# Kernel optimization log

Measured on AMD Instinct MI355X. Metric: run time of the kernel, lower is better.

Reference implementation:

```python
import jax, jax.numpy as jnp
import numpy as np

ALPHA = 1.0
STRIDE = 1
PAD = 1
DIL = 1


def setup_inputs() -> dict:
    key = jax.random.key(0)
    k1, k2, k3, k4 = jax.random.split(key, 4)
    B, C_in, C_out, H, W, K = 8, 64, 64, 128, 128, 3
    n = C_in * K * K
    stdv = 1.0 / np.sqrt(n)
    x = jax.random.normal(k1, (B, C_in, H, W), dtype=jnp.float32)
    depth = jax.random.uniform(k2, (B, 1, H, W), dtype=jnp.float32)
    weight = jax.random.uniform(k3, (C_out, C_in, K, K), dtype=jnp.float32,
                                minval=-stdv, maxval=stdv)
    bias = jax.random.uniform(k4, (C_out,), dtype=jnp.float32,
                              minval=-stdv, maxval=stdv)
    return {"x": x, "depth": depth, "weight": weight, "bias": bias}


def reference(x, depth, weight, bias):
    # Depth-guided convolution:
    #   out[b,o,p0] = bias[o] + sum_{c,k} W[o,c,k] * x[b,c,p0+pk] * exp(-alpha*|D(p0)-D(p0+pk)|)
    B, C, H, W = x.shape
    O, _, KH, KW = weight.shape
    H_out = (H + 2 * PAD - (DIL * (KH - 1) + 1)) // STRIDE + 1
    W_out = (W + 2 * PAD - (DIL * (KW - 1) + 1)) // STRIDE + 1
    x_p = jnp.pad(x, ((0, 0), (0, 0), (PAD, PAD), (PAD, PAD)))
    d_p = jnp.pad(depth, ((0, 0), (0, 0), (PAD, PAD), (PAD, PAD)))

    def tap(a, kh, kw):
        h0, w0 = kh * DIL, kw * DIL
        return a[:, :, h0:h0 + (H_out - 1) * STRIDE + 1:STRIDE,
                 w0:w0 + (W_out - 1) * STRIDE + 1:STRIDE]

    # depth at the center of each receptive field (kernel assumed odd)
    d_center = tap(d_p, KH // 2, KW // 2)  # [B,1,Ho,Wo]

    out = jnp.zeros((B, O, H_out, W_out), dtype=x.dtype)
    for kh in range(KH):
        for kw in range(KW):
            xs = tap(x_p, kh, kw)                                  # [B,C,Ho,Wo]
            ds = tap(d_p, kh, kw)                                  # [B,1,Ho,Wo]
            sim = jnp.exp(-ALPHA * jnp.abs(ds - d_center))         # [B,1,Ho,Wo]
            out = out + jnp.einsum('oc,bchw->bohw', weight[:, :, kh, kw], xs * sim)
    return out + bias[None, :, None, None]
```

## Files before the change

kernel.cpp:

```cpp
#include <hip/hip_runtime.h>

#define B_ 8
#define C_ 64
#define O_ 64
#define H_ 128
#define W_ 128

typedef __attribute__((ext_vector_type(8))) short bf16x8;
typedef __attribute__((ext_vector_type(4))) float f32x4;

__device__ __forceinline__ unsigned short f2bf(float v) {
    unsigned u = __float_as_uint(v);
    return (unsigned short)((u + 0x7FFFu + ((u >> 16) & 1u)) >> 16);
}

__device__ __forceinline__ int swz(int col) {
    return ((col ^ (col >> 3)) & 7) << 4;
}

__global__ void prep_weights(const float* __restrict__ weight,
                             unsigned short* __restrict__ wfrag) {
    int idx = blockIdx.x * 256 + threadIdx.x;
    if (idx >= 9 * 4096) return;
    int j  = idx & 7;
    int l  = (idx >> 3) & 63;
    int fi = (idx >> 9) & 3;
    int ks = (idx >> 11) & 1;
    int t  = idx >> 12;
    int o  = fi * 16 + (l & 15);
    int c  = ks * 32 + ((l >> 4) & 3) * 8 + j;
    wfrag[idx] = f2bf(weight[(o * C_ + c) * 9 + t]);
}

__global__ __launch_bounds__(256, 2)
void depthconv_mfma4(const float* __restrict__ x,
                     const float* __restrict__ depth,
                     const unsigned short* __restrict__ wfrag,
                     const float* __restrict__ bias,
                     float* __restrict__ out) {
    __shared__ __align__(16) unsigned char xs[396 * 128];
    __shared__ __align__(16) float sim[9][4][64];
    __shared__ __align__(16) float dt[6][68];

    const int tid = threadIdx.x;
    const int blk = blockIdx.x;
    const int b   = blk >> 6;
    const int rem = blk & 63;
    const int h0  = (rem >> 1) * 4;
    const int w0  = (rem & 1) * 64;

    for (int i = tid; i < 396; i += 256) {
        int r = i / 66, col = i - r * 66;
        int gh = h0 - 1 + r, gw = w0 - 1 + col;
        bool ok = ((unsigned)gh < (unsigned)H_) && ((unsigned)gw < (unsigned)W_);
        int ghc = gh < 0 ? 0 : (gh > H_ - 1 ? H_ - 1 : gh);
        int gwc = gw < 0 ? 0 : (gw > W_ - 1 ? W_ - 1 : gw);
        float v = depth[(b * H_ + ghc) * W_ + gwc];
        dt[r][col] = ok ? v : 0.f;
    }
    __syncthreads();

    const int crb = tid >> 4;
    const int q   = tid & 15;
    float4 xv[24];
    #pragma unroll
    for (int k = 0; k < 24; ++k) {
        int idx = crb + 16 * k;
        int c = idx & 63, r = idx >> 6;
        int gh  = h0 - 1 + r;
        int ghc = gh < 0 ? 0 : (gh > H_ - 1 ? H_ - 1 : gh);
        xv[k] = *(const float4*)&x[((b * C_ + c) * H_ + ghc) * W_ + w0 + q * 4];
    }
    float hv[3];
    #pragma unroll
    for (int k = 0; k < 3; ++k) {
        int i = tid + 256 * k;
        int side = i & 1, cr = i >> 1;
        int c = cr & 63, r = cr >> 6;
        int gh = h0 - 1 + r;
        int gw = side ? (w0 + 64) : (w0 - 1);
        bool ok = ((unsigned)gh < (unsigned)H_) && ((unsigned)gw < (unsigned)W_);
        int ghc = gh < 0 ? 0 : (gh > H_ - 1 ? H_ - 1 : gh);
        int gwc = gw < 0 ? 0 : (gw > W_ - 1 ? W_ - 1 : gw);
        float v = x[((b * C_ + c) * H_ + ghc) * W_ + gwc];
        hv[k] = ok ? v : 0.f;
    }

    {
        int hr = (tid >> 6) & 3, px = tid & 63;
        float dc = dt[hr + 1][px + 1];
        #pragma unroll
        for (int t = 0; t < 9; ++t) {
            const int kh = t / 3, kw = t % 3;
            sim[t][hr][px] = expf(-fabsf(dt[hr + kh][px + kw] - dc));
        }
    }

    #pragma unroll
    for (int k = 0; k < 24; ++k) {
        int idx = crb + 16 * k;
        int c = idx & 63, r = idx >> 6;
        int gh = h0 - 1 + r;
        bool okh = (unsigned)gh < (unsigned)H_;
        float vv[4] = {xv[k].x, xv[k].y, xv[k].z, xv[k].w};
        #pragma unroll
        for (int m = 0; m < 4; ++m) {
            int col = 1 + q * 4 + m;
            int rc  = r * 66 + col;
            unsigned short bv = okh ? f2bf(vv[m]) : (unsigned short)0;
            *(unsigned short*)(xs + rc * 128 + ((2 * c) ^ swz(col))) = bv;
        }
    }
    #pragma unroll
    for (int k = 0; k < 3; ++k) {
        int i = tid + 256 * k;
        int side = i & 1, cr = i >> 1;
        int c = cr & 63, r = cr >> 6;
        int col = side ? 65 : 0;
        int rc  = r * 66 + col;
        *(unsigned short*)(xs + rc * 128 + ((2 * c) ^ swz(col))) = f2bf(hv[k]);
    }
    __syncthreads();

    const int lane = tid & 63;
    const int hr   = tid >> 6;
    const int g    = lane >> 4;
    const int ln   = lane & 15;

    float acc[4][4][4];
    #pragma unroll
    for (int of = 0; of < 4; ++of) {
        float bv = bias[of * 16 + ln];
        #pragma unroll
        for (int pf = 0; pf < 4; ++pf)
            #pragma unroll
            for (int r = 0; r < 4; ++r)
                acc[pf][of][r] = bv;
    }

    #pragma unroll 1
    for (int kh = 0; kh < 3; ++kh) {
        #pragma unroll
        for (int kw = 0; kw < 3; ++kw) {
            const int t = kh * 3 + kw;
            bf16x8 bfr[2][4];
            #pragma unroll
            for (int ks = 0; ks < 2; ++ks)
                #pragma unroll
                for (int of = 0; of < 4; ++of)
                    bfr[ks][of] = *(const bf16x8*)(
                        wfrag + (((t * 2 + ks) * 4 + of) * 64 + lane) * 8);

            #pragma unroll
            for (int pf = 0; pf < 4; ++pf) {
                int col = pf * 16 + ln + kw;
                int rcb = (hr + kh) * 66 + col;
                const unsigned char* rowp = xs + rcb * 128;
                bf16x8 af0 = *(const bf16x8*)(rowp + ((2 * (g * 8))      ^ swz(col)));
                bf16x8 af1 = *(const bf16x8*)(rowp + ((2 * (32 + g * 8)) ^ swz(col)));

                f32x4 prt[4] = {};
                #pragma unroll
                for (int of = 0; of < 4; ++of)
                    prt[of] = __builtin_amdgcn_mfma_f32_16x16x32_bf16(
                        af0, bfr[0][of], prt[of], 0, 0, 0);
                #pragma unroll
                for (int of = 0; of < 4; ++of)
                    prt[of] = __builtin_amdgcn_mfma_f32_16x16x32_bf16(
                        af1, bfr[1][of], prt[of], 0, 0, 0);

                f32x4 sv = *(const f32x4*)&sim[t][hr][pf * 16 + g * 4];
                #pragma unroll
                for (int of = 0; of < 4; ++of)
                    #pragma unroll
                    for (int r = 0; r < 4; ++r)
                        acc[pf][of][r] = fmaf(sv[r], prt[of][r], acc[pf][of][r]);
            }
        }
    }

    const int h = h0 + hr;
    #pragma unroll
    for (int of = 0; of < 4; ++of) {
        int o = of * 16 + ln;
        float* dst = out + (((size_t)(b * O_ + o) * H_ + h) * W_) + w0;
        #pragma unroll
        for (int pf = 0; pf < 4; ++pf) {
            f32x4 v = { acc[pf][of][0], acc[pf][of][1],
                        acc[pf][of][2], acc[pf][of][3] };
            *(f32x4*)(dst + pf * 16 + g * 4) = v;
        }
    }
}

extern "C" void kernel_launch(void* const* d_in, const int* in_sizes, int n_in,
                              void* d_out, int out_size, void* d_ws, size_t ws_size,
                              hipStream_t stream) {
    const float* x      = (const float*)d_in[0];
    const float* depth  = (const float*)d_in[1];
    const float* weight = (const float*)d_in[2];
    const float* bias   = (const float*)d_in[3];
    float* out          = (float*)d_out;
    unsigned short* wfrag = (unsigned short*)d_ws;

    prep_weights<<<dim3(144), dim3(256), 0, stream>>>(weight, wfrag);
    depthconv_mfma4<<<dim3(512), dim3(256), 0, stream>>>(
        x, depth, wfrag, bias, out);
}
```

Measured before the change: 37.07 us.

## Halve spatial tile width, raise occupancy, pack channel pairs, remap blocks

Narrows each block's tile from 4x64 to 4x32 output pixels and doubles the grid to 1024 blocks. Launch bounds go from 2 to 4 blocks per CU, and the shared-memory footprint shrinks to match. Each thread now loads two adjacent channels and writes packed bf16x2 values to LDS. Blocks are remapped so consecutive block IDs spread across batch images, the tap loop is fully unrolled, and depth loads are issued before the x loads to overlap latency. The aim is more resident waves to hide global load latency, at the cost of more halo overhead and more redundant loads per output.

New measurement: 88.86 us. 2.4x slower.

```diff
diff --git a/kernel.cpp b/kernel.cpp
--- a/kernel.cpp
+++ b/kernel.cpp
@@ -1,4 +1,5 @@
 #include <hip/hip_runtime.h>
+#include <hip/hip_bf16.h>
 
 #define B_ 8
 #define C_ 64
@@ -32,93 +33,107 @@
     wfrag[idx] = f2bf(weight[(o * C_ + c) * 9 + t]);
 }
 
-__global__ __launch_bounds__(256, 2)
-void depthconv_mfma4(const float* __restrict__ x,
+__global__ __launch_bounds__(256, 4)
+void depthconv_mfma5(const float* __restrict__ x,
                      const float* __restrict__ depth,
                      const unsigned short* __restrict__ wfrag,
                      const float* __restrict__ bias,
                      float* __restrict__ out) {
-    __shared__ __align__(16) unsigned char xs[396 * 128];
-    __shared__ __align__(16) float sim[9][4][64];
-    __shared__ __align__(16) float dt[6][68];
+    __shared__ __align__(16) unsigned char xs[204 * 128];
+    __shared__ __align__(16) float sim[9][4][32];
+    __shared__ __align__(16) float dt[6][36];
 
     const int tid = threadIdx.x;
-    const int blk = blockIdx.x;
-    const int b   = blk >> 6;
-    const int rem = blk & 63;
-    const int h0  = (rem >> 1) * 4;
-    const int w0  = (rem & 1) * 64;
-
-    for (int i = tid; i < 396; i += 256) {
-        int r = i / 66, col = i - r * 66;
-        int gh = h0 - 1 + r, gw = w0 - 1 + col;
+    const int blk = (blockIdx.x & 7) * 128 + (blockIdx.x >> 3);
+    const int b   = blk >> 7;
+    const int rem = blk & 127;
+    const int h0  = (rem >> 2) * 4;
+    const int w0  = (rem & 3) * 32;
+
+    float dv = 0.f;
+    int dr = 0, dcol = 0;
+    if (tid < 216) {
+        dr = tid / 36; dcol = tid - dr * 36;
+        int gh = h0 - 1 + dr, gw = w0 - 1 + dcol;
         bool ok = ((unsigned)gh < (unsigned)H_) && ((unsigned)gw < (unsigned)W_);
         int ghc = gh < 0 ? 0 : (gh > H_ - 1 ? H_ - 1 : gh);
         int gwc = gw < 0 ? 0 : (gw > W_ - 1 ? W_ - 1 : gw);
         float v = depth[(b * H_ + ghc) * W_ + gwc];
-        dt[r][col] = ok ? v : 0.f;
-    }
+        dv = ok ? v : 0.f;
+    }
+
+    const int q   = tid & 7;
+    const int pcr = tid >> 3;
+    const int c0p = 2 * pcr;
+    float4 xa[6], xb[6];
+    bool okh[6];
+    #pragma unroll
+    for (int r = 0; r < 6; ++r) {
+        int gh = h0 - 1 + r;
+        okh[r] = (unsigned)gh < (unsigned)H_;
+        int ghc = gh < 0 ? 0 : (gh > H_ - 1 ? H_ - 1 : gh);
+        const float* base = &x[((b * C_ + c0p) * H_ + ghc) * W_ + w0 + q * 4];
+        xa[r] = *(const float4*)base;
+        xb[r] = *(const float4*)(base + H_ * W_);
+    }
+    float hl0[2], hl1[2];
+    int hside[2], hcp[2], hr_[2];
+    bool hok[2];
+    #pragma unroll
+    for (int k = 0; k < 2; ++k) {
+        int i = tid + 256 * k;
+        hok[k] = false;
+        if (i < 384) {
+            int side = i & 1, rp = i >> 1;
+            int cp = rp & 31, r = rp >> 5;
+            hside[k] = side; hcp[k] = cp; hr_[k] = r;
+            int gh = h0 - 1 + r;
+            int gw = side ? (w0 + 32) : (w0 - 1);
+            bool ok = ((unsigned)gh < (unsigned)H_) && ((unsigned)gw < (unsigned)W_);
+            hok[k] = true;
+            int ghc = gh < 0 ? 0 : (gh > H_ - 1 ? H_ - 1 : gh);
+            int gwc = gw < 0 ? 0 : (gw > W_ - 1 ? W_ - 1 : gw);
+            const float* p = &x[((b * C_ + 2 * cp) * H_ + ghc) * W_ + gwc];
+            float v0 = p[0], v1 = p[H_ * W_];
+            hl0[k] = ok ? v0 : 0.f;
+            hl1[k] = ok ? v1 : 0.f;
+        }
+    }
+
+    if (tid < 216) dt[dr][dcol] = dv;
     __syncthreads();
-
-    const int crb = tid >> 4;
-    const int q   = tid & 15;
-    float4 xv[24];
-    #pragma unroll
-    for (int k = 0; k < 24; ++k) {
-        int idx = crb + 16 * k;
-        int c = idx & 63, r = idx >> 6;
-        int gh  = h0 - 1 + r;
-        int ghc = gh < 0 ? 0 : (gh > H_ - 1 ? H_ - 1 : gh);
-        xv[k] = *(const float4*)&x[((b * C_ + c) * H_ + ghc) * W_ + w0 + q * 4];
-    }
-    float hv[3];
-    #pragma unroll
-    for (int k = 0; k < 3; ++k) {
-        int i = tid + 256 * k;
-        int side = i & 1, cr = i >> 1;
-        int c = cr & 63, r = cr >> 6;
-        int gh = h0 - 1 + r;
-        int gw = side ? (w0 + 64) : (w0 - 1);
-        bool ok = ((unsigned)gh < (unsigned)H_) && ((unsigned)gw < (unsigned)W_);
-        int ghc = gh < 0 ? 0 : (gh > H_ - 1 ? H_ - 1 : gh);
-        int gwc = gw < 0 ? 0 : (gw > W_ - 1 ? W_ - 1 : gw);
-        float v = x[((b * C_ + c) * H_ + ghc) * W_ + gwc];
-        hv[k] = ok ? v : 0.f;
-    }
-
-    {
-        int hr = (tid >> 6) & 3, px = tid & 63;
-        float dc = dt[hr + 1][px + 1];
-        #pragma unroll
-        for (int t = 0; t < 9; ++t) {
-            const int kh = t / 3, kw = t % 3;
-            sim[t][hr][px] = expf(-fabsf(dt[hr + kh][px + kw] - dc));
-        }
-    }
-
-    #pragma unroll
-    for (int k = 0; k < 24; ++k) {
-        int idx = crb + 16 * k;
-        int c = idx & 63, r = idx >> 6;
-        int gh = h0 - 1 + r;
-        bool okh = (unsigned)gh < (unsigned)H_;
-        float vv[4] = {xv[k].x, xv[k].y, xv[k].z, xv[k].w};
+    for (int i = tid; i < 1152; i += 256) {
+        int t  = i >> 7;
+        int hr = (i >> 5) & 3;
+        int px = i & 31;
+        int kh = t / 3, kw = t - kh * 3;
+        sim[t][hr][px] = expf(-fabsf(dt[hr + kh][px + kw] - dt[hr + 1][px + 1]));
+    }
+
+    #pragma unroll
+    for (int r = 0; r < 6; ++r) {
+        float va[4] = {xa[r].x, xa[r].y, xa[r].z, xa[r].w};
+        float vb[4] = {xb[r].x, xb[r].y, xb[r].z, xb[r].w};
         #pragma unroll
         for (int m = 0; m < 4; ++m) {
             int col = 1 + q * 4 + m;
-            int rc  = r * 66 + col;
-            unsigned short bv = okh ? f2bf(vv[m]) : (unsigned short)0;
-            *(unsigned short*)(xs + rc * 128 + ((2 * c) ^ swz(col))) = bv;
-        }
-    }
-    #pragma unroll
-    for (int k = 0; k < 3; ++k) {
-        int i = tid + 256 * k;
-        int side = i & 1, cr = i >> 1;
-        int c = cr & 63, r = cr >> 6;
-        int col = side ? 65 : 0;
-        int rc  = r * 66 + col;
-        *(unsigned short*)(xs + rc * 128 + ((2 * c) ^ swz(col))) = f2bf(hv[k]);
+            int rc  = r * 34 + col;
+            float2 pr;
+            pr.x = okh[r] ? va[m] : 0.f;
+            pr.y = okh[r] ? vb[m] : 0.f;
+            __hip_bfloat162 bv = __float22bfloat162_rn(pr);
+            *(__hip_bfloat162*)(xs + rc * 128 + ((4 * pcr) ^ swz(col))) = bv;
+        }
+    }
+    #pragma unroll
+    for (int k = 0; k < 2; ++k) {
+        if (hok[k]) {
+            int col = hside[k] ? 33 : 0;
+            int rc  = hr_[k] * 34 + col;
+            float2 pr; pr.x = hl0[k]; pr.y = hl1[k];
+            __hip_bfloat162 bv = __float22bfloat162_rn(pr);
+            *(__hip_bfloat162*)(xs + rc * 128 + ((4 * hcp[k]) ^ swz(col))) = bv;
+        }
     }
     __syncthreads();
 
@@ -127,55 +142,52 @@
     const int g    = lane >> 4;
     const int ln   = lane & 15;
 
-    float acc[4][4][4];
+    float acc[2][4][4];
     #pragma unroll
     for (int of = 0; of < 4; ++of) {
         float bv = bias[of * 16 + ln];
         #pragma unroll
-        for (int pf = 0; pf < 4; ++pf)
+        for (int pf = 0; pf < 2; ++pf)
             #pragma unroll
             for (int r = 0; r < 4; ++r)
                 acc[pf][of][r] = bv;
     }
 
-    #pragma unroll 1
-    for (int kh = 0; kh < 3; ++kh) {
-        #pragma unroll
-        for (int kw = 0; kw < 3; ++kw) {
-            const int t = kh * 3 + kw;
-            bf16x8 bfr[2][4];
-            #pragma unroll
-            for (int ks = 0; ks < 2; ++ks)
+    #pragma unroll
+    for (int t = 0; t < 9; ++t) {
+        const int kh = t / 3, kw = t - (t / 3) * 3;
+        bf16x8 bfr[2][4];
+        #pragma unroll
+        for (int ks = 0; ks < 2; ++ks)
+            #pragma unroll
+            for (int of = 0; of < 4; ++of)
+                bfr[ks][of] = *(const bf16x8*)(
+                    wfrag + (((t * 2 + ks) * 4 + of) * 64 + lane) * 8);
+
+        #pragma unroll
+        for (int pf = 0; pf < 2; ++pf) {
+            int col = pf * 16 + ln + kw;
+            int rcb = (hr + kh) * 34 + col;
+            const unsigned char* rowp = xs + rcb * 128;
+            bf16x8 af0 = *(const bf16x8*)(rowp + ((16 * g) ^ swz(col)));
+            bf16x8 af1 = *(const bf16x8*)(rowp + ((64 + 16 * g) ^ swz(col)));
+
+            f32x4 prt[4] = {};
+            #pragma unroll
+            for (int of = 0; of < 4; ++of)
+                prt[of] = __builtin_amdgcn_mfma_f32_16x16x32_bf16(
+                    af0, bfr[0][of], prt[of], 0, 0, 0);
+            #pragma unroll
+            for (int of = 0; of < 4; ++of)
+                prt[of] = __builtin_amdgcn_mfma_f32_16x16x32_bf16(
+                    af1, bfr[1][of], prt[of], 0, 0, 0);
+
+            f32x4 sv = *(const f32x4*)&sim[t][hr][pf * 16 + g * 4];
+            #pragma unroll
+            for (int of = 0; of < 4; ++of)
                 #pragma unroll
-                for (int of = 0; of < 4; ++of)
-                    bfr[ks][of] = *(const bf16x8*)(
-                        wfrag + (((t * 2 + ks) * 4 + of) * 64 + lane) * 8);
-
-            #pragma unroll
-            for (int pf = 0; pf < 4; ++pf) {
-                int col = pf * 16 + ln + kw;
-                int rcb = (hr + kh) * 66 + col;
-                const unsigned char* rowp = xs + rcb * 128;
-                bf16x8 af0 = *(const bf16x8*)(rowp + ((2 * (g * 8))      ^ swz(col)));
-                bf16x8 af1 = *(const bf16x8*)(rowp + ((2 * (32 + g * 8)) ^ swz(col)));
-
-                f32x4 prt[4] = {};
-                #pragma unroll
-                for (int of = 0; of < 4; ++of)
-                    prt[of] = __builtin_amdgcn_mfma_f32_16x16x32_bf16(
-                        af0, bfr[0][of], prt[of], 0, 0, 0);
-                #pragma unroll
-                for (int of = 0; of < 4; ++of)
-                    prt[of] = __builtin_amdgcn_mfma_f32_16x16x32_bf16(
-                        af1, bfr[1][of], prt[of], 0, 0, 0);
-
-                f32x4 sv = *(const f32x4*)&sim[t][hr][pf * 16 + g * 4];
-                #pragma unroll
-                for (int of = 0; of < 4; ++of)
-                    #pragma unroll
-                    for (int r = 0; r < 4; ++r)
-                        acc[pf][of][r] = fmaf(sv[r], prt[of][r], acc[pf][of][r]);
-            }
+                for (int r = 0; r < 4; ++r)
+                    acc[pf][of][r] = fmaf(sv[r], prt[of][r], acc[pf][of][r]);
         }
     }
 
@@ -185,7 +197,7 @@
         int o = of * 16 + ln;
         float* dst = out + (((size_t)(b * O_ + o) * H_ + h) * W_) + w0;
         #pragma unroll
-        for (int pf = 0; pf < 4; ++pf) {
+        for (int pf = 0; pf < 2; ++pf) {
             f32x4 v = { acc[pf][of][0], acc[pf][of][1],
                         acc[pf][of][2], acc[pf][of][3] };
             *(f32x4*)(dst + pf * 16 + g * 4) = v;
@@ -204,6 +216,6 @@
     unsigned short* wfrag = (unsigned short*)d_ws;
 
     prep_weights<<<dim3(144), dim3(256), 0, stream>>>(weight, wfrag);
-    depthconv_mfma4<<<dim3(512), dim3(256), 0, stream>>>(
+    depthconv_mfma5<<<dim3(1024), dim3(256), 0, stream>>>(
         x, depth, wfrag, bias, out);
 }
```

## Stage output tile through LDS for coalesced stores and pack bf16 pairs

Applied to the files above, without the earlier changes.

Shared memory becomes one 64KB arena that holds the input tile, sim and depth, and is reused at the end to stage the output accumulators. Threads then write full contiguous 256-byte rows per output channel and row, where before they issued scattered 16-byte stores. The x staging now loads channel pairs and converts them with a packed bf16x2 conversion, writing 4-byte LDS stores instead of 2-byte ones. The costs are a larger LDS footprint, which may limit the 2-blocks-per-CU occupancy, and extra barriers plus an LDS round trip in the epilogue.

After: 36.59 us. Within noise of the previous version (-1.3%).

```diff
diff --git a/kernel.cpp b/kernel.cpp
--- a/kernel.cpp
+++ b/kernel.cpp
@@ -1,4 +1,5 @@
 #include <hip/hip_runtime.h>
+#include <hip/hip_bf16.h>
 
 #define B_ 8
 #define C_ 64
@@ -33,14 +34,15 @@
 }
 
 __global__ __launch_bounds__(256, 2)
-void depthconv_mfma4(const float* __restrict__ x,
+void depthconv_mfma6(const float* __restrict__ x,
                      const float* __restrict__ depth,
                      const unsigned short* __restrict__ wfrag,
                      const float* __restrict__ bias,
                      float* __restrict__ out) {
-    __shared__ __align__(16) unsigned char xs[396 * 128];
-    __shared__ __align__(16) float sim[9][4][64];
-    __shared__ __align__(16) float dt[6][68];
+    __shared__ __align__(16) unsigned char arena[65536];
+    unsigned char* xs   = arena;
+    float (*sim)[4][64] = (float (*)[4][64])(arena + 50688);
+    float (*dt)[68]     = (float (*)[68])(arena + 59904);
 
     const int tid = threadIdx.x;
     const int blk = blockIdx.x;
@@ -60,65 +62,81 @@
     }
     __syncthreads();
 
-    const int crb = tid >> 4;
-    const int q   = tid & 15;
-    float4 xv[24];
-    #pragma unroll
-    for (int k = 0; k < 24; ++k) {
-        int idx = crb + 16 * k;
-        int c = idx & 63, r = idx >> 6;
-        int gh  = h0 - 1 + r;
-        int ghc = gh < 0 ? 0 : (gh > H_ - 1 ? H_ - 1 : gh);
-        xv[k] = *(const float4*)&x[((b * C_ + c) * H_ + ghc) * W_ + w0 + q * 4];
-    }
-    float hv[3];
-    #pragma unroll
-    for (int k = 0; k < 3; ++k) {
+    const int q  = tid & 15;
+    const int pc = tid >> 4;
+    float4 xa[12], xb[12];
+    #pragma unroll
+    for (int k = 0; k < 12; ++k) {
+        int r    = k >> 1;
+        int pair = pc + 16 * (k & 1);
+        int gh   = h0 - 1 + r;
+        int ghc  = gh < 0 ? 0 : (gh > H_ - 1 ? H_ - 1 : gh);
+        const float* base = &x[((b * C_ + 2 * pair) * H_ + ghc) * W_ + w0 + q * 4];
+        xa[k] = *(const float4*)base;
+        xb[k] = *(const float4*)(base + H_ * W_);
+    }
+    float hl0[2], hl1[2];
+    int hside[2], hpair[2], hr_[2];
+    bool hact[2];
+    #pragma unroll
+    for (int k = 0; k < 2; ++k) {
         int i = tid + 256 * k;
-        int side = i & 1, cr = i >> 1;
-        int c = cr & 63, r = cr >> 6;
-        int gh = h0 - 1 + r;
-        int gw = side ? (w0 + 64) : (w0 - 1);
-        bool ok = ((unsigned)gh < (unsigned)H_) && ((unsigned)gw < (unsigned)W_);
-        int ghc = gh < 0 ? 0 : (gh > H_ - 1 ? H_ - 1 : gh);
-        int gwc = gw < 0 ? 0 : (gw > W_ - 1 ? W_ - 1 : gw);
-        float v = x[((b * C_ + c) * H_ + ghc) * W_ + gwc];
-        hv[k] = ok ? v : 0.f;
+        hact[k] = false;
+        if (i < 384) {
+            int side = i & 1, rp = i >> 1;
+            int pair = rp & 31, r = rp >> 5;
+            hside[k] = side; hpair[k] = pair; hr_[k] = r;
+            hact[k] = true;
+            int gh = h0 - 1 + r;
+            int gw = side ? (w0 + 64) : (w0 - 1);
+            bool ok = ((unsigned)gh < (unsigned)H_) && ((unsigned)gw < (unsigned)W_);
+            int ghc = gh < 0 ? 0 : (gh > H_ - 1 ? H_ - 1 : gh);
+            int gwc = gw < 0 ? 0 : (gw > W_ - 1 ? W_ - 1 : gw);
+            const float* p = &x[((b * C_ + 2 * pair) * H_ + ghc) * W_ + gwc];
+            float v0 = p[0], v1 = p[H_ * W_];
+            hl0[k] = ok ? v0 : 0.f;
+            hl1[k] = ok ? v1 : 0.f;
+        }
     }
 
     {
-        int hr = (tid >> 6) & 3, px = tid & 63;
-        float dc = dt[hr + 1][px + 1];
+        int shr = (tid >> 6) & 3, px = tid & 63;
+        float dc = dt[shr + 1][px + 1];
         #pragma unroll
         for (int t = 0; t < 9; ++t) {
             const int kh = t / 3, kw = t % 3;
-            sim[t][hr][px] = expf(-fabsf(dt[hr + kh][px + kw] - dc));
-        }
-    }
-
-    #pragma unroll
-    for (int k = 0; k < 24; ++k) {
-        int idx = crb + 16 * k;
-        int c = idx & 63, r = idx >> 6;
-        int gh = h0 - 1 + r;
+            sim[t][shr][px] = expf(-fabsf(dt[shr + kh][px + kw] - dc));
+        }
+    }
+
+    #pragma unroll
+    for (int k = 0; k < 12; ++k) {
+        int r    = k >> 1;
+        int pair = pc + 16 * (k & 1);
+        int gh   = h0 - 1 + r;
         bool okh = (unsigned)gh < (unsigned)H_;
-        float vv[4] = {xv[k].x, xv[k].y, xv[k].z, xv[k].w};
+        float va[4] = {xa[k].x, xa[k].y, xa[k].z, xa[k].w};
+        float vb[4] = {xb[k].x, xb[k].y, xb[k].z, xb[k].w};
         #pragma unroll
         for (int m = 0; m < 4; ++m) {
             int col = 1 + q * 4 + m;
             int rc  = r * 66 + col;
-            unsigned short bv = okh ? f2bf(vv[m]) : (unsigned short)0;
-            *(unsigned short*)(xs + rc * 128 + ((2 * c) ^ swz(col))) = bv;
-        }
-    }
-    #pragma unroll
-    for (int k = 0; k < 3; ++k) {
-        int i = tid + 256 * k;
-        int side = i & 1, cr = i >> 1;
-        int c = cr & 63, r = cr >> 6;
-        int col = side ? 65 : 0;
-        int rc  = r * 66 + col;
-        *(unsigned short*)(xs + rc * 128 + ((2 * c) ^ swz(col))) = f2bf(hv[k]);
+            float2 pr;
+            pr.x = okh ? va[m] : 0.f;
+            pr.y = okh ? vb[m] : 0.f;
+            __hip_bfloat162 bv = __float22bfloat162_rn(pr);
+            *(__hip_bfloat162*)(xs + rc * 128 + ((4 * pair) ^ swz(col))) = bv;
+        }
+    }
+    #pragma unroll
+    for (int k = 0; k < 2; ++k) {
+        if (hact[k]) {
+            int col = hside[k] ? 65 : 0;
+            int rc  = hr_[k] * 66 + col;
+            float2 pr; pr.x = hl0[k]; pr.y = hl1[k];
+            __hip_bfloat162 bv = __float22bfloat162_rn(pr);
+            *(__hip_bfloat162*)(xs + rc * 128 + ((4 * hpair[k]) ^ swz(col))) = bv;
+        }
     }
     __syncthreads();
 
@@ -156,8 +174,8 @@
                 int col = pf * 16 + ln + kw;
                 int rcb = (hr + kh) * 66 + col;
                 const unsigned char* rowp = xs + rcb * 128;
-                bf16x8 af0 = *(const bf16x8*)(rowp + ((2 * (g * 8))      ^ swz(col)));
-                bf16x8 af1 = *(const bf16x8*)(rowp + ((2 * (32 + g * 8)) ^ swz(col)));
+                bf16x8 af0 = *(const bf16x8*)(rowp + ((16 * g) ^ swz(col)));
+                bf16x8 af1 = *(const bf16x8*)(rowp + ((64 + 16 * g) ^ swz(col)));
 
                 f32x4 prt[4] = {};
                 #pragma unroll
@@ -179,17 +197,28 @@
         }
     }
 
-    const int h = h0 + hr;
-    #pragma unroll
-    for (int of = 0; of < 4; ++of) {
-        int o = of * 16 + ln;
-        float* dst = out + (((size_t)(b * O_ + o) * H_ + h) * W_) + w0;
-        #pragma unroll
-        for (int pf = 0; pf < 4; ++pf) {
+    __syncthreads();
+    #pragma unroll
+    for (int pf = 0; pf < 4; ++pf)
+        #pragma unroll
+        for (int of = 0; of < 4; ++of) {
+            int rowid = ((of * 16 + ln) << 2) + hr;
+            int chunk = (pf << 2) + g;
             f32x4 v = { acc[pf][of][0], acc[pf][of][1],
                         acc[pf][of][2], acc[pf][of][3] };
-            *(f32x4*)(dst + pf * 16 + g * 4) = v;
-        }
+            *(f32x4*)(arena + rowid * 256 + ((chunk ^ ln) << 4)) = v;
+        }
+    __syncthreads();
+    #pragma unroll
+    for (int m = 0; m < 16; ++m) {
+        int idx   = m * 256 + tid;
+        int rowid = idx >> 4;
+        int cc    = idx & 15;
+        int key   = (rowid >> 2) & 15;
+        f32x4 v = *(const f32x4*)(arena + rowid * 256 + ((cc ^ key) << 4));
+        int o  = rowid >> 2;
+        int hh = rowid & 3;
+        *(f32x4*)(out + (((size_t)(b * O_ + o) * H_ + h0 + hh) * W_) + w0 + cc * 4) = v;
     }
 }
 
@@ -204,6 +233,6 @@
     unsigned short* wfrag = (unsigned short*)d_ws;
 
     prep_weights<<<dim3(144), dim3(256), 0, stream>>>(weight, wfrag);
-    depthconv_mfma4<<<dim3(512), dim3(256), 0, stream>>>(
+    depthconv_mfma6<<<dim3(512), dim3(256), 0, stream>>>(
         x, depth, wfrag, bias, out);
 }
```

## Split 64-wide tile into two 32-wide halves with prefetch of second half

Applied to the files above, without the earlier changes.

Each block now stages its 64-column tile in two 32-column halves through a smaller shared buffer. The second half's global loads are issued before the first half's MFMA compute, so load latency overlaps with math. Channels are packed in pairs and written as bf16x2 to shared memory. The smaller LDS footprint may allow more resident blocks, at the cost of an extra barrier, the weight fragments being reloaded per half, and more live registers for the prefetched data.

After: 44.09 us. +18.9%, slower.

```diff
diff --git a/kernel.cpp b/kernel.cpp
--- a/kernel.cpp
+++ b/kernel.cpp
@@ -1,10 +1,12 @@
 #include <hip/hip_runtime.h>
+#include <hip/hip_bf16.h>
 
 #define B_ 8
 #define C_ 64
 #define O_ 64
 #define H_ 128
 #define W_ 128
+#define HW_ (H_ * W_)
 
 typedef __attribute__((ext_vector_type(8))) short bf16x8;
 typedef __attribute__((ext_vector_type(4))) float f32x4;
@@ -13,9 +15,11 @@
     unsigned u = __float_as_uint(v);
     return (unsigned short)((u + 0x7FFFu + ((u >> 16) & 1u)) >> 16);
 }
-
 __device__ __forceinline__ int swz(int col) {
     return ((col ^ (col >> 3)) & 7) << 4;
+}
+__device__ __forceinline__ int clampi(int v, int lo, int hi) {
+    return v < lo ? lo : (v > hi ? hi : v);
 }
 
 __global__ void prep_weights(const float* __restrict__ weight,
@@ -32,163 +36,246 @@
     wfrag[idx] = f2bf(weight[(o * C_ + c) * 9 + t]);
 }
 
+template<int SB>
+__device__ __forceinline__ void compute_tile(
+    const unsigned char* xs, const float (&sim)[9][4][64],
+    const unsigned short* __restrict__ wfrag,
+    int hr, int g, int ln, int lane, float (&acc)[2][4][4]) {
+    #pragma unroll 1
+    for (int kh = 0; kh < 3; ++kh) {
+        #pragma unroll
+        for (int kw = 0; kw < 3; ++kw) {
+            const int t = kh * 3 + kw;
+            bf16x8 bfr[2][4];
+            #pragma unroll
+            for (int ks = 0; ks < 2; ++ks)
+                #pragma unroll
+                for (int of = 0; of < 4; ++of)
+                    bfr[ks][of] = *(const bf16x8*)(
+                        wfrag + (((t * 2 + ks) * 4 + of) * 64 + lane) * 8);
+
+            #pragma unroll
+            for (int pf = 0; pf < 2; ++pf) {
+                int col = pf * 16 + ln + kw;
+                const unsigned char* rowp = xs + ((hr + kh) * 34 + col) * 128;
+                bf16x8 af0 = *(const bf16x8*)(rowp + ((16 * g) ^ swz(col)));
+                bf16x8 af1 = *(const bf16x8*)(rowp + ((64 + 16 * g) ^ swz(col)));
+
+                f32x4 prt[4] = {};
+                #pragma unroll
+                for (int of = 0; of < 4; ++of)
+                    prt[of] = __builtin_amdgcn_mfma_f32_16x16x32_bf16(
+                        af0, bfr[0][of], prt[of], 0, 0, 0);
+                #pragma unroll
+                for (int of = 0; of < 4; ++of)
+                    prt[of] = __builtin_amdgcn_mfma_f32_16x16x32_bf16(
+                        af1, bfr[1][of], prt[of], 0, 0, 0);
+
+                f32x4 sv = *(const f32x4*)&sim[t][hr][SB + pf * 16 + g * 4];
+                #pragma unroll
+                for (int of = 0; of < 4; ++of)
+                    #pragma unroll
+                    for (int r = 0; r < 4; ++r)
+                        acc[pf][of][r] = fmaf(sv[r], prt[of][r], acc[pf][of][r]);
+            }
+        }
+    }
+}
+
 __global__ __launch_bounds__(256, 2)
-void depthconv_mfma4(const float* __restrict__ x,
+void depthconv_mfma8(const float* __restrict__ x,
                      const float* __restrict__ depth,
                      const unsigned short* __restrict__ wfrag,
                      const float* __restrict__ bias,
                      float* __restrict__ out) {
-    __shared__ __align__(16) unsigned char xs[396 * 128];
+    __shared__ __align__(16) unsigned char xs[204 * 128];
     __shared__ __align__(16) float sim[9][4][64];
     __shared__ __align__(16) float dt[6][68];
 
-    const int tid = threadIdx.x;
-    const int blk = blockIdx.x;
-    const int b   = blk >> 6;
-    const int rem = blk & 63;
-    const int h0  = (rem >> 1) * 4;
-    const int w0  = (rem & 1) * 64;
+    const int tid  = threadIdx.x;
+    const int blk  = blockIdx.x;
+    const int wp   = blk & 1;
+    const int rg   = blk >> 1;
+    const int h0   = (rg & 31) * 4;
+    const int b    = rg >> 5;
+    const int base = wp * 64;
 
     for (int i = tid; i < 396; i += 256) {
         int r = i / 66, col = i - r * 66;
-        int gh = h0 - 1 + r, gw = w0 - 1 + col;
+        int gh = h0 - 1 + r, gw = base - 1 + col;
         bool ok = ((unsigned)gh < (unsigned)H_) && ((unsigned)gw < (unsigned)W_);
-        int ghc = gh < 0 ? 0 : (gh > H_ - 1 ? H_ - 1 : gh);
-        int gwc = gw < 0 ? 0 : (gw > W_ - 1 ? W_ - 1 : gw);
-        float v = depth[(b * H_ + ghc) * W_ + gwc];
+        float v = depth[(b * H_ + clampi(gh, 0, H_ - 1)) * W_ + clampi(gw, 0, W_ - 1)];
         dt[r][col] = ok ? v : 0.f;
     }
     __syncthreads();
 
-    const int crb = tid >> 4;
-    const int q   = tid & 15;
-    float4 xv[24];
-    #pragma unroll
-    for (int k = 0; k < 24; ++k) {
-        int idx = crb + 16 * k;
-        int c = idx & 63, r = idx >> 6;
-        int gh  = h0 - 1 + r;
-        int ghc = gh < 0 ? 0 : (gh > H_ - 1 ? H_ - 1 : gh);
-        xv[k] = *(const float4*)&x[((b * C_ + c) * H_ + ghc) * W_ + w0 + q * 4];
-    }
-    float hv[3];
-    #pragma unroll
-    for (int k = 0; k < 3; ++k) {
-        int i = tid + 256 * k;
-        int side = i & 1, cr = i >> 1;
-        int c = cr & 63, r = cr >> 6;
-        int gh = h0 - 1 + r;
-        int gw = side ? (w0 + 64) : (w0 - 1);
-        bool ok = ((unsigned)gh < (unsigned)H_) && ((unsigned)gw < (unsigned)W_);
-        int ghc = gh < 0 ? 0 : (gh > H_ - 1 ? H_ - 1 : gh);
-        int gwc = gw < 0 ? 0 : (gw > W_ - 1 ? W_ - 1 : gw);
-        float v = x[((b * C_ + c) * H_ + ghc) * W_ + gwc];
-        hv[k] = ok ? v : 0.f;
+    const int q  = tid & 7;
+    const int pc = tid >> 3;
+
+    float4 xa[6], xb[6];
+    #pragma unroll
+    for (int r = 0; r < 6; ++r) {
+        int ghc = clampi(h0 - 1 + r, 0, H_ - 1);
+        const float* p = &x[((b * C_ + 2 * pc) * H_ + ghc) * W_ + base + q * 4];
+        xa[r] = *(const float4*)p;
+        xb[r] = *(const float4*)(p + HW_);
+    }
+    float ha[2][2];
+    #pragma unroll
+    for (int k = 0; k < 2; ++k) {
+        int i = tid + 256 * k;
+        if (i < 384) {
+            int side = i & 1, pair = (i >> 1) & 31, r = i >> 6;
+            int gh = h0 - 1 + r;
+            int gw = side ? base + 32 : base - 1;
+            bool ok = ((unsigned)gh < (unsigned)H_) && ((unsigned)gw < (unsigned)W_);
+            const float* p = &x[((b * C_ + 2 * pair) * H_ + clampi(gh, 0, H_ - 1)) * W_
+                                + clampi(gw, 0, W_ - 1)];
+            float v0 = p[0], v1 = p[HW_];
+            ha[k][0] = ok ? v0 : 0.f;
+            ha[k][1] = ok ? v1 : 0.f;
+        }
     }
 
     {
-        int hr = (tid >> 6) & 3, px = tid & 63;
-        float dc = dt[hr + 1][px + 1];
+        int sr = tid >> 6, px = tid & 63;
         #pragma unroll
         for (int t = 0; t < 9; ++t) {
             const int kh = t / 3, kw = t % 3;
-            sim[t][hr][px] = expf(-fabsf(dt[hr + kh][px + kw] - dc));
-        }
-    }
-
-    #pragma unroll
-    for (int k = 0; k < 24; ++k) {
-        int idx = crb + 16 * k;
-        int c = idx & 63, r = idx >> 6;
+            sim[t][sr][px] = expf(-fabsf(dt[sr + kh][px + kw] - dt[sr + 1][px + 1]));
+        }
+    }
+
+    #pragma unroll
+    for (int r = 0; r < 6; ++r) {
         int gh = h0 - 1 + r;
         bool okh = (unsigned)gh < (unsigned)H_;
-        float vv[4] = {xv[k].x, xv[k].y, xv[k].z, xv[k].w};
+        float va[4] = {xa[r].x, xa[r].y, xa[r].z, xa[r].w};
+        float vb[4] = {xb[r].x, xb[r].y, xb[r].z, xb[r].w};
         #pragma unroll
         for (int m = 0; m < 4; ++m) {
             int col = 1 + q * 4 + m;
-            int rc  = r * 66 + col;
-            unsigned short bv = okh ? f2bf(vv[m]) : (unsigned short)0;
-            *(unsigned short*)(xs + rc * 128 + ((2 * c) ^ swz(col))) = bv;
-        }
-    }
-    #pragma unroll
-    for (int k = 0; k < 3; ++k) {
-        int i = tid + 256 * k;
-        int side = i & 1, cr = i >> 1;
-        int c = cr & 63, r = cr >> 6;
-        int col = side ? 65 : 0;
-        int rc  = r * 66 + col;
-        *(unsigned short*)(xs + rc * 128 + ((2 * c) ^ swz(col))) = f2bf(hv[k]);
-    }
-    __syncthreads();
+            float2 pr;
+            pr.x = okh ? va[m] : 0.f;
+            pr.y = okh ? vb[m] : 0.f;
+            __hip_bfloat162 bv = __float22bfloat162_rn(pr);
+            *(__hip_bfloat162*)(xs + (r * 34 + col) * 128 + ((4 * pc) ^ swz(col))) = bv;
+        }
+    }
+    #pragma unroll
+    for (int k = 0; k < 2; ++k) {
+        int i = tid + 256 * k;
+        if (i < 384) {
+            int side = i & 1, pair = (i >> 1) & 31, r = i >> 6;
+            int col = side ? 33 : 0;
+            float2 pr; pr.x = ha[k][0]; pr.y = ha[k][1];
+            __hip_bfloat162 bv = __float22bfloat162_rn(pr);
+            *(__hip_bfloat162*)(xs + (r * 34 + col) * 128 + ((4 * pair) ^ swz(col))) = bv;
+        }
+    }
+    __syncthreads();
+
+    float4 ya[6], yb[6];
+    #pragma unroll
+    for (int r = 0; r < 6; ++r) {
+        int ghc = clampi(h0 - 1 + r, 0, H_ - 1);
+        const float* p = &x[((b * C_ + 2 * pc) * H_ + ghc) * W_ + base + 32 + q * 4];
+        ya[r] = *(const float4*)p;
+        yb[r] = *(const float4*)(p + HW_);
+    }
+    float hb[2][2];
+    #pragma unroll
+    for (int k = 0; k < 2; ++k) {
+        int i = tid + 256 * k;
+        if (i < 384) {
+            int side = i & 1, pair = (i >> 1) & 31, r = i >> 6;
+            int gh = h0 - 1 + r;
+            int gw = side ? base + 64 : base + 31;
+            bool ok = ((unsigned)gh < (unsigned)H_) && ((unsigned)gw < (unsigned)W_);
+            const float* p = &x[((b * C_ + 2 * pair) * H_ + clampi(gh, 0, H_ - 1)) * W_
+                                + clampi(gw, 0, W_ - 1)];
+            float v0 = p[0], v1 = p[HW_];
+            hb[k][0] = ok ? v0 : 0.f;
+            hb[k][1] = ok ? v1 : 0.f;
+        }
+    }
+    __builtin_amdgcn_sched_barrier(0);
 
     const int lane = tid & 63;
     const int hr   = tid >> 6;
     const int g    = lane >> 4;
     const int ln   = lane & 15;
 
-    float acc[4][4][4];
+    float accA[2][4][4];
     #pragma unroll
     for (int of = 0; of < 4; ++of) {
         float bv = bias[of * 16 + ln];
         #pragma unroll
-        for (int pf = 0; pf < 4; ++pf)
+        for (int pf = 0; pf < 2; ++pf)
             #pragma unroll
             for (int r = 0; r < 4; ++r)
-                acc[pf][of][r] = bv;
-    }
-
-    #pragma unroll 1
-    for (int kh = 0; kh < 3; ++kh) {
-        #pragma unroll
-        for (int kw = 0; kw < 3; ++kw) {
-            const int t = kh * 3 + kw;
-            bf16x8 bfr[2][4];
-            #pragma unroll
-            for (int ks = 0; ks < 2; ++ks)
-                #pragma unroll
-                for (int of = 0; of < 4; ++of)
-                    bfr[ks][of] = *(const bf16x8*)(
-                        wfrag + (((t * 2 + ks) * 4 + of) * 64 + lane) * 8);
-
-            #pragma unroll
-            for (int pf = 0; pf < 4; ++pf) {
-                int col = pf * 16 + ln + kw;
-                int rcb = (hr + kh) * 66 + col;
-                const unsigned char* rowp = xs + rcb * 128;
-                bf16x8 af0 = *(const bf16x8*)(rowp + ((2 * (g * 8))      ^ swz(col)));
-                bf16x8 af1 = *(const bf16x8*)(rowp + ((2 * (32 + g * 8)) ^ swz(col)));
-
-                f32x4 prt[4] = {};
-                #pragma unroll
-                for (int of = 0; of < 4; ++of)
-                    prt[of] = __builtin_amdgcn_mfma_f32_16x16x32_bf16(
-                        af0, bfr[0][of], prt[of], 0, 0, 0);
-                #pragma unroll
-                for (int of = 0; of < 4; ++of)
-                    prt[of] = __builtin_amdgcn_mfma_f32_16x16x32_bf16(
-                        af1, bfr[1][of], prt[of], 0, 0, 0);
-
-                f32x4 sv = *(const f32x4*)&sim[t][hr][pf * 16 + g * 4];
-                #pragma unroll
-                for (int of = 0; of < 4; ++of)
-                    #pragma unroll
-                    for (int r = 0; r < 4; ++r)
-                        acc[pf][of][r] = fmaf(sv[r], prt[of][r], acc[pf][of][r]);
-            }
-        }
-    }
+                accA[pf][of][r] = bv;
+    }
+    compute_tile<0>(xs, sim, wfrag, hr, g, ln, lane, accA);
+    __syncthreads();
+
+    #pragma unroll
+    for (int r = 0; r < 6; ++r) {
+        int gh = h0 - 1 + r;
+        bool okh = (unsigned)gh < (unsigned)H_;
+        float va[4] = {ya[r].x, ya[r].y, ya[r].z, ya[r].w};
+        float vb[4] = {yb[r].x, yb[r].y, yb[r].z, yb[r].w};
+        #pragma unroll
+        for (int m = 0; m < 4; ++m) {
+            int col = 1 + q * 4 + m;
+            float2 pr;
+            pr.x = okh ? va[m] : 0.f;
+            pr.y = okh ? vb[m] : 0.f;
+            __hip_bfloat162 bv = __float22bfloat162_rn(pr);
+            *(__hip_bfloat162*)(xs + (r * 34 + col) * 128 + ((4 * pc) ^ swz(col))) = bv;
+        }
+    }
+    #pragma unroll
+    for (int k = 0; k < 2; ++k) {
+        int i = tid + 256 * k;
+        if (i < 384) {
+            int side = i & 1, pair = (i >> 1) & 31, r = i >> 6;
+            int col = side ? 33 : 0;
+            float2 pr; pr.x = hb[k][0]; pr.y = hb[k][1];
+            __hip_bfloat162 bv = __float22bfloat162_rn(pr);
+            *(__hip_bfloat162*)(xs + (r * 34 + col) * 128 + ((4 * pair) ^ swz(col))) = bv;
+        }
+    }
+    __syncthreads();
+
+    float accB[2][4][4];
+    #pragma unroll
+    for (int of = 0; of < 4; ++of) {
+        float bv = bias[of * 16 + ln];
+        #pragma unroll
+        for (int pf = 0; pf < 2; ++pf)
+            #pragma unroll
+            for (int r = 0; r < 4; ++r)
+                accB[pf][of][r] = bv;
+    }
+    compute_tile<32>(xs, sim, wfrag, hr, g, ln, lane, accB);
 
     const int h = h0 + hr;
     #pragma unroll
     for (int of = 0; of < 4; ++of) {
         int o = of * 16 + ln;
-        float* dst = out + (((size_t)(b * O_ + o) * H_ + h) * W_) + w0;
-        #pragma unroll
-        for (int pf = 0; pf < 4; ++pf) {
-            f32x4 v = { acc[pf][of][0], acc[pf][of][1],
-                        acc[pf][of][2], acc[pf][of][3] };
+        float* dst = out + (((size_t)(b * O_ + o) * H_ + h) * W_) + base;
+        #pragma unroll
+        for (int pf = 0; pf < 2; ++pf) {
+            f32x4 v = { accA[pf][of][0], accA[pf][of][1],
+                        accA[pf][of][2], accA[pf][of][3] };
             *(f32x4*)(dst + pf * 16 + g * 4) = v;
+        }
+        #pragma unroll
+        for (int pf = 0; pf < 2; ++pf) {
+            f32x4 v = { accB[pf][of][0], accB[pf][of][1],
+                        accB[pf][of][2], accB[pf][of][3] };
+            *(f32x4*)(dst + 32 + pf * 16 + g * 4) = v;
         }
     }
 }
@@ -204,6 +291,6 @@
     unsigned short* wfrag = (unsigned short*)d_ws;
 
     prep_weights<<<dim3(144), dim3(256), 0, stream>>>(weight, wfrag);
-    depthconv_mfma4<<<dim3(512), dim3(256), 0, stream>>>(
+    depthconv_mfma8<<<dim3(512), dim3(256), 0, stream>>>(
         x, depth, wfrag, bias, out);
 }
```
